# Kernel optimization log

Hardware: AMD Instinct MI355X
Metric: run time of the kernel (lower is better)

The kernel has to match this reference:

```python
import jax, jax.numpy as jnp
import numpy as np

LEAK = 0.2
N, C, T, H, DOUT = 512, 16, 15, 32, 32


def setup_inputs() -> dict:
    key = jax.random.key(0)
    k = jax.random.split(key, 5)
    x = jax.random.normal(k[0], (N, C), dtype=jnp.float32)
    adj = jax.random.uniform(k[1], (N, N, T), dtype=jnp.float32)
    W1 = jax.random.normal(k[2], (2 * C, T + 1, H), dtype=jnp.float32) * 0.05
    W2 = jax.random.normal(k[3], (2 * C, T + 1, DOUT), dtype=jnp.float32) * 0.05
    W3 = jax.random.normal(k[4], (C, H), dtype=jnp.float32) * 0.05
    return {"x": x, "adj": adj, "W1": W1, "W2": W2, "W3": W3}


def reference(x, adj, W1, W2, W3):
    n, c = x.shape
    # input_diag: [N,N,C,1], diagonal copy of node features
    diag = jnp.einsum('mn,ni->mni', jnp.eye(n, dtype=x.dtype), x)[..., None]
    # D = concat(adj-weighted broadcast of x, diag) along edge-type axis -> [N,N,C,T+1]
    D = jnp.concatenate([jnp.einsum('mnt,ni->mnit', adj, x), diag], axis=3)
    # symmetrize along channel axis -> [N,N,2C,T+1]
    D = jnp.concatenate([D, jnp.transpose(D, (1, 0, 2, 3))], axis=2)
    K = jnp.einsum('mnit,ith->mnh', D, W1)   # [N,N,H]
    V = jnp.einsum('mnit,itd->mnd', D, W2)   # [N,N,DOUT]
    Q = x @ W3                               # [N,H]
    logits1 = jnp.einsum('nh,nmh->nm', Q, K)
    logits2 = jnp.einsum('mh,nmh->nm', Q, K)
    s1 = jax.nn.softmax(logits1, axis=1)
    s2 = jax.nn.softmax(logits2, axis=0)
    temp = jnp.einsum('nm,nmd->nd', s1, V) + jnp.einsum('nm,nmd->md', s2, V)
    return jnp.maximum(temp, LEAK * temp)  # lrelu
```

## Files before the change

### kernel.cpp

```cpp
#include <hip/hip_runtime.h>
#include <hip/hip_bf16.h>

#define NNODE 512
#define CCH   16
#define TT    15
#define TP    16
#define HH    32
#define DD    32

typedef unsigned short u16;
typedef unsigned int   u32;
typedef short bf8 __attribute__((ext_vector_type(8)));
typedef float f4  __attribute__((ext_vector_type(4)));

__device__ __forceinline__ float bf2f(u16 v) {
    union { u32 u; float f; } x; x.u = ((u32)v) << 16; return x.f;
}
__device__ __forceinline__ u16 f2bf(float f) {
    union { float f; u32 u; } x; x.f = f;
    u32 u = x.u;
    return (u16)((u + 0x7FFFu + ((u >> 16) & 1u)) >> 16);
}
__device__ __forceinline__ void unpack8(uint4 p, float* o) {
    o[0]=bf2f((u16)(p.x & 0xffffu)); o[1]=bf2f((u16)(p.x >> 16));
    o[2]=bf2f((u16)(p.y & 0xffffu)); o[3]=bf2f((u16)(p.y >> 16));
    o[4]=bf2f((u16)(p.z & 0xffffu)); o[5]=bf2f((u16)(p.z >> 16));
    o[6]=bf2f((u16)(p.w & 0xffffu)); o[7]=bf2f((u16)(p.w >> 16));
}
__device__ __forceinline__ uint4 pack8(const u16* v) {
    return make_uint4((u32)v[0]|((u32)v[1]<<16), (u32)v[2]|((u32)v[3]<<16),
                      (u32)v[4]|((u32)v[5]<<16), (u32)v[6]|((u32)v[7]<<16));
}

__global__ __launch_bounds__(256) void k_prep_adjp(
    const float* __restrict__ x, const float* __restrict__ W1,
    const float* __restrict__ W2, const float* __restrict__ W3,
    const float* __restrict__ adj,
    u16* __restrict__ A1, u16* __restrict__ B1,
    u16* __restrict__ A2T, u16* __restrict__ B2T,
    u16* __restrict__ Qb, float* __restrict__ QAd, float* __restrict__ QB,
    u16* __restrict__ adjP, u16* __restrict__ adjPT,
    float* __restrict__ temp, float* __restrict__ u1, float* __restrict__ v2)
{
    int tid = threadIdx.x;
    if (blockIdx.x >= 768) {
        int idx = (blockIdx.x - 768) * 256 + tid;
        if (idx < 16384) temp[idx] = 0.f;
        else if (idx < 24576) u1[idx - 16384] = 0.f;
        else if (idx < 32768) v2[idx - 24576] = 0.f;
        return;
    }
    if (blockIdx.x < 512) {
        int n = blockIdx.x;
        __shared__ alignas(16) float xs[CCH];
        __shared__ alignas(16) float A1row[512], B1row[512];
        __shared__ alignas(16) float A2row[512], B2row[512];
        __shared__ alignas(16) float Qs[HH];
        if (tid < CCH) xs[tid] = x[n*CCH + tid];
        __syncthreads();
        float xr[CCH];
        #pragma unroll
        for (int i=0;i<CCH;i++) xr[i]=xs[i];
        #pragma unroll
        for (int rep=0; rep<2; rep++) {
            int c = tid + rep*256;
            float a1=0.f,b1=0.f,a2=0.f,b2=0.f;
            #pragma unroll
            for (int i=0;i<CCH;i++) {
                a1 += xr[i]*W1[i*512 + c];
                b1 += xr[i]*W1[(CCH+i)*512 + c];
                a2 += xr[i]*W2[i*512 + c];
                b2 += xr[i]*W2[(CCH+i)*512 + c];
            }
            A1[(size_t)n*512 + c]=f2bf(a1); B1[(size_t)n*512 + c]=f2bf(b1);
            A1row[c]=a1; B1row[c]=b1; A2row[c]=a2; B2row[c]=b2;
        }
        if (tid < HH) {
            float q=0.f;
            #pragma unroll
            for (int i=0;i<CCH;i++) q += xr[i]*W3[i*HH + tid];
            Qs[tid]=q; Qb[(size_t)n*HH + tid]=f2bf(q);
        }
        __syncthreads();
        if (tid < TP) {
            float qa=0.f, qb=0.f;
            #pragma unroll
            for (int h=0;h<HH;h++) { qa += Qs[h]*A1row[tid*HH+h]; qb += Qs[h]*B1row[tid*HH+h]; }
            QAd[(size_t)n*TP + tid]=qa; QB[(size_t)n*TP + tid]=qb;
        }
        {
            int d = tid >> 3, t0 = (tid & 7) * 2;
            u32 pa = (u32)f2bf(A2row[t0*32 + d]) | ((u32)f2bf(A2row[(t0+1)*32 + d]) << 16);
            u32 pb = (u32)f2bf(B2row[t0*32 + d]) | ((u32)f2bf(B2row[(t0+1)*32 + d]) << 16);
            *(u32*)(A2T + (size_t)d*8192 + n*16 + t0) = pa;
            *(u32*)(B2T + (size_t)d*8192 + n*16 + t0) = pb;
        }
    } else {
        int b = blockIdx.x - 512;
        int n0 = (b >> 4) * 32, m0 = (b & 15) * 32;
        __shared__ alignas(16) u16 s[32*520];
        #pragma unroll
        for (int i = 0; i < 60; i++) {
            int e = tid + i*256;
            int nl = e / 480; int rem = e - nl*480;
            int ml = rem / 15; int t = rem - ml*15;
            float v = adj[((size_t)(n0+nl)*512 + (m0+ml))*TT + t];
            s[nl*520 + ml*16 + t] = f2bf(v);
        }
        #pragma unroll
        for (int i = 0; i < 4; i++) {
            int e = tid + i*256; int nl = e >> 5, ml = e & 31;
            s[nl*520 + ml*16 + 15] = ((n0+nl) == (m0+ml)) ? (u16)0x3F80 : (u16)0;
        }
        __syncthreads();
        #pragma unroll
        for (int i = 0; i < 8; i++) {
            int c = tid + i*256;
            int nl = c >> 6, off = (c & 63) * 8;
            uint4 vv = *(const uint4*)(s + nl*520 + off);
            *(uint4*)(adjP + (size_t)(n0+nl)*8192 + m0*16 + off) = vv;
        }
        #pragma unroll
        for (int i = 0; i < 8; i++) {
            int c = tid + i*256;
            int ml = c >> 6, nlh = c & 63, nl = nlh >> 1, half = nlh & 1;
            uint4 vv = *(const uint4*)(s + nl*520 + ml*16 + half*8);
            *(uint4*)(adjPT + (size_t)(m0+ml)*8192 + (n0+nl)*16 + half*8) = vv;
        }
    }
}

__global__ __launch_bounds__(256) void k_logits(
    const u16* __restrict__ Qb, const u16* __restrict__ A1, const u16* __restrict__ B1,
    const u16* __restrict__ adjP, const u16* __restrict__ adjPT,
    const float* __restrict__ QAd, const float* __restrict__ QB,
    float* __restrict__ L1, float* __restrict__ L2T,
    float2* __restrict__ statsP)
{
    const int m0 = blockIdx.x * 16, n0 = blockIdx.y * 16;
    const int tid = threadIdx.x;
    const int wv = tid >> 6, lane = tid & 63, l15 = lane & 15, quad = lane >> 4;
    __shared__ alignas(16) float sL1[16*17];
    __shared__ alignas(16) float sL2[16*17];

    bf8 qbN = *(const bf8*)(Qb + (size_t)(n0 + l15)*32 + quad*8);
    bf8 qbM = *(const bf8*)(Qb + (size_t)(m0 + l15)*32 + quad*8);
    float4 qb4 = *(const float4*)(QB  + (size_t)(n0 + l15)*TP + quad*4);
    float4 qa4 = *(const float4*)(QAd + (size_t)(m0 + l15)*TP + quad*4);

    #pragma unroll
    for (int j = 0; j < 4; j++) {
        int m = m0 + wv*4 + j;
        bf8 aA1 = *(const bf8*)(A1 + (size_t)m*512 + l15*32 + quad*8);
        f4 z = {0.f,0.f,0.f,0.f};
        f4 g = __builtin_amdgcn_mfma_f32_16x16x32_bf16(aA1, qbN, z, 0, 0, 0);
        uint2 ax = *(const uint2*)(adjPT + (size_t)m*8192 + (n0 + l15)*16 + quad*4);
        uint2 ay = *(const uint2*)(adjP  + (size_t)m*8192 + (n0 + l15)*16 + quad*4);
        float v;
        v = bf2f((u16)(ax.x & 0xffffu)) * g[0];
        v = fmaf(bf2f((u16)(ax.x >> 16)),     g[1], v);
        v = fmaf(bf2f((u16)(ax.y & 0xffffu)), g[2], v);
        v = fmaf(bf2f((u16)(ax.y >> 16)),     g[3], v);
        v = fmaf(bf2f((u16)(ay.x & 0xffffu)), qb4.x, v);
        v = fmaf(bf2f((u16)(ay.x >> 16)),     qb4.y, v);
        v = fmaf(bf2f((u16)(ay.y & 0xffffu)), qb4.z, v);
        v = fmaf(bf2f((u16)(ay.y >> 16)),     qb4.w, v);
        v += __shfl_xor(v, 16, 64);
        v += __shfl_xor(v, 32, 64);
        if (quad == 0) sL1[l15*17 + wv*4 + j] = v;
    }
    #pragma unroll
    for (int j = 0; j < 4; j++) {
        int n = n0 + wv*4 + j;
        bf8 aB1 = *(const bf8*)(B1 + (size_t)n*512 + l15*32 + quad*8);
        f4 z = {0.f,0.f,0.f,0.f};
        f4 h = __builtin_amdgcn_mfma_f32_16x16x32_bf16(aB1, qbM, z, 0, 0, 0);
        uint2 ax = *(const uint2*)(adjPT + (size_t)n*8192 + (m0 + l15)*16 + quad*4);
        uint2 ay = *(const uint2*)(adjP  + (size_t)n*8192 + (m0 + l15)*16 + quad*4);
        float v;
        v = bf2f((u16)(ax.x & 0xffffu)) * h[0];
        v = fmaf(bf2f((u16)(ax.x >> 16)),     h[1], v);
        v = fmaf(bf2f((u16)(ax.y & 0xffffu)), h[2], v);
        v = fmaf(bf2f((u16)(ax.y >> 16)),     h[3], v);
        v = fmaf(bf2f((u16)(ay.x & 0xffffu)), qa4.x, v);
        v = fmaf(bf2f((u16)(ay.x >> 16)),     qa4.y, v);
        v = fmaf(bf2f((u16)(ay.y & 0xffffu)), qa4.z, v);
        v = fmaf(bf2f((u16)(ay.y >> 16)),     qa4.w, v);
        v += __shfl_xor(v, 16, 64);
        v += __shfl_xor(v, 32, 64);
        if (quad == 0) sL2[l15*17 + wv*4 + j] = v;
    }
    __syncthreads();
    int row = tid >> 4, col = tid & 15;
    float v1 = sL1[row*17+col];
    float v2v = sL2[row*17+col];
    L1 [(size_t)(n0+row)*NNODE + m0 + col] = v1;
    L2T[(size_t)(m0+row)*NNODE + n0 + col] = v2v;

    float mx1 = v1, mx2 = v2v;
    #pragma unroll
    for (int o=1; o<16; o<<=1) {
        mx1 = fmaxf(mx1, __shfl_xor(mx1, o, 64));
        mx2 = fmaxf(mx2, __shfl_xor(mx2, o, 64));
    }
    float s1 = __expf(v1 - mx1), s2 = __expf(v2v - mx2);
    #pragma unroll
    for (int o=1; o<16; o<<=1) {
        s1 += __shfl_xor(s1, o, 64);
        s2 += __shfl_xor(s2, o, 64);
    }
    if (col == 0) {
        float2 st1; st1.x = mx1; st1.y = s1;
        float2 st2; st2.x = mx2; st2.y = s2;
        statsP[(size_t)(n0+row)*32 + blockIdx.x]         = st1;
        statsP[(size_t)(NNODE + m0+row)*32 + blockIdx.y] = st2;
    }
}

__global__ __launch_bounds__(256) void k_smx_gemm(
    const float* __restrict__ L1, const float* __restrict__ L2T,
    const u16* __restrict__ adjP, const u16* __restrict__ adjPT,
    const u16* __restrict__ A2T, const u16* __restrict__ B2T,
    const float2* __restrict__ statsP,
    float* __restrict__ temp, float* __restrict__ u1, float* __restrict__ v2)
{
    const int j0 = blockIdx.x * 16, kc = blockIdx.y, dir = blockIdx.z;
    const int tid = threadIdx.x;
    const int wv = tid >> 6, lane = tid & 63, l15 = lane & 15, quad = lane >> 4;
    const float* Lbase = dir ? L2T : L1;

    __shared__ alignas(16) u16 Wt[16*256];
    __shared__ alignas(16) float redb[4][512];
    __shared__ float2 sst[16];

    {
        int j = tid >> 4, pp = tid & 15;
        const float2* sp = statsP + (size_t)(dir*NNODE + j0 + j)*32;
        float2 a = sp[pp*2], b = sp[pp*2+1];
        float mx = fmaxf(a.x, b.x);
        float sm = a.y*__expf(a.x - mx) + b.y*__expf(b.x - mx);
        #pragma unroll
        for (int o=1; o<16; o<<=1) {
            float omx = __shfl_xor(mx, o, 64), osm = __shfl_xor(sm, o, 64);
            float nmx = fmaxf(mx, omx);
            sm = sm*__expf(mx - nmx) + osm*__expf(omx - nmx);
            mx = nmx;
        }
        if (pp == 0) { float2 st; st.x = mx; st.y = 1.0f/sm; sst[j] = st; }
    }
    __syncthreads();

    {
        int j = tid >> 4, cb = tid & 15;
        int m = kc*16 + cb;
        float2 st = sst[j];
        float s0 = __expf(Lbase[(size_t)(j0+j)*NNODE + m] - st.x) * st.y;

        const uint4* pp = (const uint4*)(adjP + (size_t)(j0+j)*8192 + m*16);
        float av[16]; unpack8(pp[0], av); unpack8(pp[1], av+8);
        u16 wo[16];
        #pragma unroll
        for (int e=0;e<16;e++) wo[e] = f2bf(s0*av[e]);
        #pragma unroll
        for (int q=0;q<2;q++) {
            int sl = (cb*2 + q) ^ (j & 7);
            *(uint4*)&Wt[j*256 + sl*8] = pack8(wo + q*8);
        }

        const uint4* qq = (const uint4*)(adjPT + (size_t)(j0+j)*8192 + m*16);
        float tv[16]; unpack8(qq[0], tv); unpack8(qq[1], tv+8);
        float ut[16];
        #pragma unroll
        for (int t=0;t<16;t++) ut[t] = s0*tv[t];
        #pragma unroll
        for (int i=0;i<8;i++) {
            float v0 = (lane&1) ? ut[i] : ut[i+8];
            float r0 = __shfl_xor(v0, 1, 64);
            ut[i] = ((lane&1) ? ut[i+8] : ut[i]) + r0;
        }
        #pragma unroll
        for (int i=0;i<4;i++) {
            float v0 = (lane&2) ? ut[i] : ut[i+4];
            float r0 = __shfl_xor(v0, 2, 64);
            ut[i] = ((lane&2) ? ut[i+4] : ut[i]) + r0;
        }
        #pragma unroll
        for (int i=0;i<2;i++) {
            float v0 = (lane&4) ? ut[i] : ut[i+2];
            float r0 = __shfl_xor(v0, 4, 64);
            ut[i] = ((lane&4) ? ut[i+2] : ut[i]) + r0;
        }
        {
            float v0 = (lane&8) ? ut[0] : ut[1];
            float r0 = __shfl_xor(v0, 8, 64);
            ut[0] = ((lane&8) ? ut[1] : ut[0]) + r0;
        }
        int tm = ((cb&1)<<3) | ((cb&2)<<1) | ((cb&4)>>1) | ((cb&8)>>3);
        atomicAdd((dir ? v2 : u1) + (size_t)(j0+j)*TP + tm, ut[0]);
    }
    __syncthreads();

    {
        const u16* Bmat = dir ? B2T : A2T;
        f4 acc0 = {0.f,0.f,0.f,0.f}, acc1 = {0.f,0.f,0.f,0.f};
        #pragma unroll
        for (int st2 = 0; st2 < 2; st2++) {
            int s = wv*2 + st2;
            bf8 afr = *(const bf8*)&Wt[l15*256 + (((s*4 + quad) ^ (l15 & 7)) << 3)];
            bf8 b0 = *(const bf8*)(Bmat + (size_t)(l15)*8192    + kc*256 + s*32 + quad*8);
            bf8 b1 = *(const bf8*)(Bmat + (size_t)(16+l15)*8192 + kc*256 + s*32 + quad*8);
            acc0 = __builtin_amdgcn_mfma_f32_16x16x32_bf16(afr, b0, acc0, 0, 0, 0);
            acc1 = __builtin_amdgcn_mfma_f32_16x16x32_bf16(afr, b1, acc1, 0, 0, 0);
        }
        #pragma unroll
        for (int r = 0; r < 4; r++) {
            redb[wv][      (quad*4+r)*16 + l15] = acc0[r];
            redb[wv][256 + (quad*4+r)*16 + l15] = acc1[r];
        }
    }
    __syncthreads();
    #pragma unroll
    for (int h = 0; h < 2; h++) {
        int o = tid + h*256;
        int jj = o >> 5, d = o & 31;
        int idx = (d >> 4)*256 + jj*16 + (d & 15);
        float v = redb[0][idx] + redb[1][idx] + redb[2][idx] + redb[3][idx];
        atomicAdd(&temp[(size_t)(j0 + jj)*DD + d], v);
    }
}

__global__ __launch_bounds__(256) void k_final(
    const float* __restrict__ temp, const float* __restrict__ u1, const float* __restrict__ v2,
    const u16* __restrict__ A2T, const u16* __restrict__ B2T, float* __restrict__ out)
{
    int base = blockIdx.x * 256 + threadIdx.x;
    int j = base >> 5, d = base & 31;
    float acc = temp[(size_t)j*DD + d];
    const uint4* pb2 = (const uint4*)(B2T + (size_t)d*8192 + j*16);
    const uint4* pa2 = (const uint4*)(A2T + (size_t)d*8192 + j*16);
    float bv[16], avv[16];
    unpack8(pb2[0], bv);  unpack8(pb2[1], bv+8);
    unpack8(pa2[0], avv); unpack8(pa2[1], avv+8);
    #pragma unroll
    for (int t = 0; t < 16; t++)
        acc += u1[(size_t)j*TP + t]*bv[t] + v2[(size_t)j*TP + t]*avv[t];
    out[(size_t)j*DD + d] = fmaxf(acc, 0.2f*acc);
}

extern "C" void kernel_launch(void* const* d_in, const int* in_sizes, int n_in,
                              void* d_out, int out_size, void* d_ws, size_t ws_size,
                              hipStream_t stream)
{
    (void)in_sizes; (void)n_in; (void)out_size; (void)ws_size;
    const float* x   = (const float*)d_in[0];
    const float* adj = (const float*)d_in[1];
    const float* W1  = (const float*)d_in[2];
    const float* W2  = (const float*)d_in[3];
    const float* W3  = (const float*)d_in[4];

    char* ws = (char*)d_ws;
    u16*   adjP  = (u16*)(ws);
    u16*   adjPT = (u16*)(ws + 0x800000);
    u16*   A1    = (u16*)(ws + 0x1000000);
    u16*   B1    = (u16*)(ws + 0x1080000);
    u16*   A2T   = (u16*)(ws + 0x1100000);
    u16*   B2T   = (u16*)(ws + 0x1180000);
    u16*   Qb    = (u16*)(ws + 0x1200000);
    float* QAd   = (float*)(ws + 0x1210000);
    float* QB    = (float*)(ws + 0x1220000);
    float* L1    = (float*)(ws + 0x1300000);
    float* L2T   = (float*)(ws + 0x1400000);
    float* temp  = (float*)(ws + 0x1500000);
    float* u1    = (float*)(ws + 0x1510000);
    float* v2    = (float*)(ws + 0x1520000);
    float2* statsP=(float2*)(ws + 0x1530000);

    k_prep_adjp<<<896, 256, 0, stream>>>(x, W1, W2, W3, adj,
                                         A1, B1, A2T, B2T, Qb, QAd, QB, adjP, adjPT,
                                         temp, u1, v2);
    k_logits<<<dim3(32,32), 256, 0, stream>>>(Qb, A1, B1, adjP, adjPT, QAd, QB,
                                              L1, L2T, statsP);
    k_smx_gemm<<<dim3(32,32,2), 256, 0, stream>>>(L1, L2T, adjP, adjPT, A2T, B2T,
                                                  statsP, temp, u1, v2);
    k_final<<<64, 256, 0, stream>>>(temp, u1, v2, A2T, B2T, (float*)d_out);
}
```

Baseline: 102.2 us.

## Fuse softmax directions in GEMM kernel, widen logits tiles, shrink prep tiles

The softmax-weighted GEMM kernel now does both directions in one block. It reads adjP/adjPT and the logits once, builds two weight tiles, and accumulates both A2T and B2T products into the same accumulators, which halves grid size and cuts the atomic adds to temp. The logits kernel now covers 32 n-rows per block so the m-side Q fragments and QAd are reused, and the stats layout is adjusted to match. The adj-permute blocks in prep use 16-row tiles, which doubles their block count. The cost is more registers and LDS per block and lower parallelism in the fused kernels.

```diff
diff --git a/kernel.cpp b/kernel.cpp
--- a/kernel.cpp
+++ b/kernel.cpp
@@ -43,8 +43,8 @@
     float* __restrict__ temp, float* __restrict__ u1, float* __restrict__ v2)
 {
     int tid = threadIdx.x;
-    if (blockIdx.x >= 768) {
-        int idx = (blockIdx.x - 768) * 256 + tid;
+    if (blockIdx.x >= 1024) {
+        int idx = (blockIdx.x - 1024) * 256 + tid;
         if (idx < 16384) temp[idx] = 0.f;
         else if (idx < 24576) u1[idx - 16384] = 0.f;
         else if (idx < 32768) v2[idx - 24576] = 0.f;
@@ -97,10 +97,10 @@
         }
     } else {
         int b = blockIdx.x - 512;
-        int n0 = (b >> 4) * 32, m0 = (b & 15) * 32;
-        __shared__ alignas(16) u16 s[32*520];
-        #pragma unroll
-        for (int i = 0; i < 60; i++) {
+        int n0 = (b >> 4) * 16, m0 = (b & 15) * 32;
+        __shared__ alignas(16) u16 s[16*520];
+        #pragma unroll
+        for (int i = 0; i < 30; i++) {
             int e = tid + i*256;
             int nl = e / 480; int rem = e - nl*480;
             int ml = rem / 15; int t = rem - ml*15;
@@ -108,22 +108,22 @@
             s[nl*520 + ml*16 + t] = f2bf(v);
         }
         #pragma unroll
-        for (int i = 0; i < 4; i++) {
+        for (int i = 0; i < 2; i++) {
             int e = tid + i*256; int nl = e >> 5, ml = e & 31;
             s[nl*520 + ml*16 + 15] = ((n0+nl) == (m0+ml)) ? (u16)0x3F80 : (u16)0;
         }
         __syncthreads();
         #pragma unroll
-        for (int i = 0; i < 8; i++) {
+        for (int i = 0; i < 4; i++) {
             int c = tid + i*256;
             int nl = c >> 6, off = (c & 63) * 8;
             uint4 vv = *(const uint4*)(s + nl*520 + off);
             *(uint4*)(adjP + (size_t)(n0+nl)*8192 + m0*16 + off) = vv;
         }
         #pragma unroll
-        for (int i = 0; i < 8; i++) {
+        for (int i = 0; i < 4; i++) {
             int c = tid + i*256;
-            int ml = c >> 6, nlh = c & 63, nl = nlh >> 1, half = nlh & 1;
+            int ml = c >> 5, nlh = c & 31, nl = nlh >> 1, half = nlh & 1;
             uint4 vv = *(const uint4*)(s + nl*520 + ml*16 + half*8);
             *(uint4*)(adjPT + (size_t)(m0+ml)*8192 + (n0+nl)*16 + half*8) = vv;
         }
@@ -137,41 +137,62 @@
     float* __restrict__ L1, float* __restrict__ L2T,
     float2* __restrict__ statsP)
 {
-    const int m0 = blockIdx.x * 16, n0 = blockIdx.y * 16;
+    const int m0 = blockIdx.x * 16, n0 = blockIdx.y * 32;
     const int tid = threadIdx.x;
     const int wv = tid >> 6, lane = tid & 63, l15 = lane & 15, quad = lane >> 4;
-    __shared__ alignas(16) float sL1[16*17];
-    __shared__ alignas(16) float sL2[16*17];
-
-    bf8 qbN = *(const bf8*)(Qb + (size_t)(n0 + l15)*32 + quad*8);
-    bf8 qbM = *(const bf8*)(Qb + (size_t)(m0 + l15)*32 + quad*8);
-    float4 qb4 = *(const float4*)(QB  + (size_t)(n0 + l15)*TP + quad*4);
-    float4 qa4 = *(const float4*)(QAd + (size_t)(m0 + l15)*TP + quad*4);
+    __shared__ alignas(16) float sL1[32*17];
+    __shared__ alignas(16) float sL2[16*33];
+
+    bf8 qbN0 = *(const bf8*)(Qb + (size_t)(n0 + l15)*32 + quad*8);
+    bf8 qbN1 = *(const bf8*)(Qb + (size_t)(n0 + 16 + l15)*32 + quad*8);
+    bf8 qbM  = *(const bf8*)(Qb + (size_t)(m0 + l15)*32 + quad*8);
+    float4 qb40 = *(const float4*)(QB  + (size_t)(n0 + l15)*TP + quad*4);
+    float4 qb41 = *(const float4*)(QB  + (size_t)(n0 + 16 + l15)*TP + quad*4);
+    float4 qa4  = *(const float4*)(QAd + (size_t)(m0 + l15)*TP + quad*4);
 
     #pragma unroll
     for (int j = 0; j < 4; j++) {
         int m = m0 + wv*4 + j;
         bf8 aA1 = *(const bf8*)(A1 + (size_t)m*512 + l15*32 + quad*8);
         f4 z = {0.f,0.f,0.f,0.f};
-        f4 g = __builtin_amdgcn_mfma_f32_16x16x32_bf16(aA1, qbN, z, 0, 0, 0);
-        uint2 ax = *(const uint2*)(adjPT + (size_t)m*8192 + (n0 + l15)*16 + quad*4);
-        uint2 ay = *(const uint2*)(adjP  + (size_t)m*8192 + (n0 + l15)*16 + quad*4);
-        float v;
-        v = bf2f((u16)(ax.x & 0xffffu)) * g[0];
-        v = fmaf(bf2f((u16)(ax.x >> 16)),     g[1], v);
-        v = fmaf(bf2f((u16)(ax.y & 0xffffu)), g[2], v);
-        v = fmaf(bf2f((u16)(ax.y >> 16)),     g[3], v);
-        v = fmaf(bf2f((u16)(ay.x & 0xffffu)), qb4.x, v);
-        v = fmaf(bf2f((u16)(ay.x >> 16)),     qb4.y, v);
-        v = fmaf(bf2f((u16)(ay.y & 0xffffu)), qb4.z, v);
-        v = fmaf(bf2f((u16)(ay.y >> 16)),     qb4.w, v);
-        v += __shfl_xor(v, 16, 64);
-        v += __shfl_xor(v, 32, 64);
-        if (quad == 0) sL1[l15*17 + wv*4 + j] = v;
-    }
-    #pragma unroll
-    for (int j = 0; j < 4; j++) {
-        int n = n0 + wv*4 + j;
+        f4 g0 = __builtin_amdgcn_mfma_f32_16x16x32_bf16(aA1, qbN0, z, 0, 0, 0);
+        f4 g1 = __builtin_amdgcn_mfma_f32_16x16x32_bf16(aA1, qbN1, z, 0, 0, 0);
+        {
+            uint2 ax = *(const uint2*)(adjPT + (size_t)m*8192 + (n0 + l15)*16 + quad*4);
+            uint2 ay = *(const uint2*)(adjP  + (size_t)m*8192 + (n0 + l15)*16 + quad*4);
+            float v;
+            v = bf2f((u16)(ax.x & 0xffffu)) * g0[0];
+            v = fmaf(bf2f((u16)(ax.x >> 16)),     g0[1], v);
+            v = fmaf(bf2f((u16)(ax.y & 0xffffu)), g0[2], v);
+            v = fmaf(bf2f((u16)(ax.y >> 16)),     g0[3], v);
+            v = fmaf(bf2f((u16)(ay.x & 0xffffu)), qb40.x, v);
+            v = fmaf(bf2f((u16)(ay.x >> 16)),     qb40.y, v);
+            v = fmaf(bf2f((u16)(ay.y & 0xffffu)), qb40.z, v);
+            v = fmaf(bf2f((u16)(ay.y >> 16)),     qb40.w, v);
+            v += __shfl_xor(v, 16, 64);
+            v += __shfl_xor(v, 32, 64);
+            if (quad == 0) sL1[l15*17 + wv*4 + j] = v;
+        }
+        {
+            uint2 ax = *(const uint2*)(adjPT + (size_t)m*8192 + (n0 + 16 + l15)*16 + quad*4);
+            uint2 ay = *(const uint2*)(adjP  + (size_t)m*8192 + (n0 + 16 + l15)*16 + quad*4);
+            float v;
+            v = bf2f((u16)(ax.x & 0xffffu)) * g1[0];
+            v = fmaf(bf2f((u16)(ax.x >> 16)),     g1[1], v);
+            v = fmaf(bf2f((u16)(ax.y & 0xffffu)), g1[2], v);
+            v = fmaf(bf2f((u16)(ax.y >> 16)),     g1[3], v);
+            v = fmaf(bf2f((u16)(ay.x & 0xffffu)), qb41.x, v);
+            v = fmaf(bf2f((u16)(ay.x >> 16)),     qb41.y, v);
+            v = fmaf(bf2f((u16)(ay.y & 0xffffu)), qb41.z, v);
+            v = fmaf(bf2f((u16)(ay.y >> 16)),     qb41.w, v);
+            v += __shfl_xor(v, 16, 64);
+            v += __shfl_xor(v, 32, 64);
+            if (quad == 0) sL1[(16 + l15)*17 + wv*4 + j] = v;
+        }
+    }
+    #pragma unroll
+    for (int j2 = 0; j2 < 8; j2++) {
+        int n = n0 + wv*8 + j2;
         bf8 aB1 = *(const bf8*)(B1 + (size_t)n*512 + l15*32 + quad*8);
         f4 z = {0.f,0.f,0.f,0.f};
         f4 h = __builtin_amdgcn_mfma_f32_16x16x32_bf16(aB1, qbM, z, 0, 0, 0);
@@ -188,32 +209,38 @@
         v = fmaf(bf2f((u16)(ay.y >> 16)),     qa4.w, v);
         v += __shfl_xor(v, 16, 64);
         v += __shfl_xor(v, 32, 64);
-        if (quad == 0) sL2[l15*17 + wv*4 + j] = v;
+        if (quad == 0) sL2[l15*33 + wv*8 + j2] = v;
     }
     __syncthreads();
+
     int row = tid >> 4, col = tid & 15;
-    float v1 = sL1[row*17+col];
-    float v2v = sL2[row*17+col];
-    L1 [(size_t)(n0+row)*NNODE + m0 + col] = v1;
-    L2T[(size_t)(m0+row)*NNODE + n0 + col] = v2v;
-
-    float mx1 = v1, mx2 = v2v;
-    #pragma unroll
-    for (int o=1; o<16; o<<=1) {
-        mx1 = fmaxf(mx1, __shfl_xor(mx1, o, 64));
-        mx2 = fmaxf(mx2, __shfl_xor(mx2, o, 64));
-    }
-    float s1 = __expf(v1 - mx1), s2 = __expf(v2v - mx2);
-    #pragma unroll
-    for (int o=1; o<16; o<<=1) {
-        s1 += __shfl_xor(s1, o, 64);
-        s2 += __shfl_xor(s2, o, 64);
-    }
-    if (col == 0) {
-        float2 st1; st1.x = mx1; st1.y = s1;
-        float2 st2; st2.x = mx2; st2.y = s2;
-        statsP[(size_t)(n0+row)*32 + blockIdx.x]         = st1;
-        statsP[(size_t)(NNODE + m0+row)*32 + blockIdx.y] = st2;
+    #pragma unroll
+    for (int rr = 0; rr < 2; rr++) {
+        int r = rr*16 + row;
+        float v1 = sL1[r*17 + col];
+        L1[(size_t)(n0+r)*NNODE + m0 + col] = v1;
+        float mx = v1;
+        #pragma unroll
+        for (int o=1; o<16; o<<=1) mx = fmaxf(mx, __shfl_xor(mx, o, 64));
+        float s1 = __expf(v1 - mx);
+        #pragma unroll
+        for (int o=1; o<16; o<<=1) s1 += __shfl_xor(s1, o, 64);
+        if (col == 0) { float2 st; st.x = mx; st.y = s1;
+                        statsP[(size_t)(n0+r)*32 + blockIdx.x] = st; }
+    }
+    #pragma unroll
+    for (int cc = 0; cc < 2; cc++) {
+        int c2 = cc*16 + col;
+        float v2v = sL2[row*33 + c2];
+        L2T[(size_t)(m0+row)*NNODE + n0 + c2] = v2v;
+        float mx = v2v;
+        #pragma unroll
+        for (int o=1; o<16; o<<=1) mx = fmaxf(mx, __shfl_xor(mx, o, 64));
+        float s2 = __expf(v2v - mx);
+        #pragma unroll
+        for (int o=1; o<16; o<<=1) s2 += __shfl_xor(s2, o, 64);
+        if (col == 0) { float2 st; st.x = mx; st.y = s2;
+                        statsP[(size_t)(NNODE + m0+row)*32 + blockIdx.y*2 + cc] = st; }
     }
 }
 
@@ -224,93 +251,126 @@
     const float2* __restrict__ statsP,
     float* __restrict__ temp, float* __restrict__ u1, float* __restrict__ v2)
 {
-    const int j0 = blockIdx.x * 16, kc = blockIdx.y, dir = blockIdx.z;
+    const int j0 = blockIdx.x * 16, kc = blockIdx.y;
     const int tid = threadIdx.x;
     const int wv = tid >> 6, lane = tid & 63, l15 = lane & 15, quad = lane >> 4;
-    const float* Lbase = dir ? L2T : L1;
-
-    __shared__ alignas(16) u16 Wt[16*256];
+
+    __shared__ alignas(16) u16 Wt0[16*256];
+    __shared__ alignas(16) u16 Wt1[16*256];
     __shared__ alignas(16) float redb[4][512];
-    __shared__ float2 sst[16];
+    __shared__ float2 sst0[16], sst1[16];
 
     {
         int j = tid >> 4, pp = tid & 15;
-        const float2* sp = statsP + (size_t)(dir*NNODE + j0 + j)*32;
-        float2 a = sp[pp*2], b = sp[pp*2+1];
-        float mx = fmaxf(a.x, b.x);
-        float sm = a.y*__expf(a.x - mx) + b.y*__expf(b.x - mx);
-        #pragma unroll
-        for (int o=1; o<16; o<<=1) {
-            float omx = __shfl_xor(mx, o, 64), osm = __shfl_xor(sm, o, 64);
-            float nmx = fmaxf(mx, omx);
-            sm = sm*__expf(mx - nmx) + osm*__expf(omx - nmx);
-            mx = nmx;
-        }
-        if (pp == 0) { float2 st; st.x = mx; st.y = 1.0f/sm; sst[j] = st; }
+        {
+            const float2* sp = statsP + (size_t)(j0 + j)*32;
+            float2 a = sp[pp*2], b = sp[pp*2+1];
+            float mx = fmaxf(a.x, b.x);
+            float sm = a.y*__expf(a.x - mx) + b.y*__expf(b.x - mx);
+            #pragma unroll
+            for (int o=1; o<16; o<<=1) {
+                float omx = __shfl_xor(mx, o, 64), osm = __shfl_xor(sm, o, 64);
+                float nmx = fmaxf(mx, omx);
+                sm = sm*__expf(mx - nmx) + osm*__expf(omx - nmx);
+                mx = nmx;
+            }
+            if (pp == 0) { float2 st; st.x = mx; st.y = 1.0f/sm; sst0[j] = st; }
+        }
+        {
+            const float2* sp = statsP + (size_t)(NNODE + j0 + j)*32;
+            float2 a = sp[pp*2], b = sp[pp*2+1];
+            float mx = fmaxf(a.x, b.x);
+            float sm = a.y*__expf(a.x - mx) + b.y*__expf(b.x - mx);
+            #pragma unroll
+            for (int o=1; o<16; o<<=1) {
+                float omx = __shfl_xor(mx, o, 64), osm = __shfl_xor(sm, o, 64);
+                float nmx = fmaxf(mx, omx);
+                sm = sm*__expf(mx - nmx) + osm*__expf(omx - nmx);
+                mx = nmx;
+            }
+            if (pp == 0) { float2 st; st.x = mx; st.y = 1.0f/sm; sst1[j] = st; }
+        }
     }
     __syncthreads();
 
     {
         int j = tid >> 4, cb = tid & 15;
         int m = kc*16 + cb;
-        float2 st = sst[j];
-        float s0 = __expf(Lbase[(size_t)(j0+j)*NNODE + m] - st.x) * st.y;
-
-        const uint4* pp = (const uint4*)(adjP + (size_t)(j0+j)*8192 + m*16);
-        float av[16]; unpack8(pp[0], av); unpack8(pp[1], av+8);
-        u16 wo[16];
-        #pragma unroll
-        for (int e=0;e<16;e++) wo[e] = f2bf(s0*av[e]);
+        float2 st0 = sst0[j], st1 = sst1[j];
+        float s0 = __expf(L1 [(size_t)(j0+j)*NNODE + m] - st0.x) * st0.y;
+        float s1 = __expf(L2T[(size_t)(j0+j)*NNODE + m] - st1.x) * st1.y;
+
+        const uint4* pp4 = (const uint4*)(adjP + (size_t)(j0+j)*8192 + m*16);
+        float av[16]; unpack8(pp4[0], av); unpack8(pp4[1], av+8);
+        u16 wo0[16], wo1[16];
+        #pragma unroll
+        for (int e=0;e<16;e++) { wo0[e] = f2bf(s0*av[e]); wo1[e] = f2bf(s1*av[e]); }
         #pragma unroll
         for (int q=0;q<2;q++) {
             int sl = (cb*2 + q) ^ (j & 7);
-            *(uint4*)&Wt[j*256 + sl*8] = pack8(wo + q*8);
+            *(uint4*)&Wt0[j*256 + sl*8] = pack8(wo0 + q*8);
+            *(uint4*)&Wt1[j*256 + sl*8] = pack8(wo1 + q*8);
         }
 
         const uint4* qq = (const uint4*)(adjPT + (size_t)(j0+j)*8192 + m*16);
         float tv[16]; unpack8(qq[0], tv); unpack8(qq[1], tv+8);
-        float ut[16];
-        #pragma unroll
-        for (int t=0;t<16;t++) ut[t] = s0*tv[t];
+        float ut0[16], ut1[16];
+        #pragma unroll
+        for (int t=0;t<16;t++) { ut0[t] = s0*tv[t]; ut1[t] = s1*tv[t]; }
         #pragma unroll
         for (int i=0;i<8;i++) {
-            float v0 = (lane&1) ? ut[i] : ut[i+8];
-            float r0 = __shfl_xor(v0, 1, 64);
-            ut[i] = ((lane&1) ? ut[i+8] : ut[i]) + r0;
+            float a0 = (lane&1) ? ut0[i] : ut0[i+8];
+            float a1 = (lane&1) ? ut1[i] : ut1[i+8];
+            float r0 = __shfl_xor(a0, 1, 64), r1 = __shfl_xor(a1, 1, 64);
+            ut0[i] = ((lane&1) ? ut0[i+8] : ut0[i]) + r0;
+            ut1[i] = ((lane&1) ? ut1[i+8] : ut1[i]) + r1;
         }
         #pragma unroll
         for (int i=0;i<4;i++) {
-            float v0 = (lane&2) ? ut[i] : ut[i+4];
-            float r0 = __shfl_xor(v0, 2, 64);
-            ut[i] = ((lane&2) ? ut[i+4] : ut[i]) + r0;
+            float a0 = (lane&2) ? ut0[i] : ut0[i+4];
+            float a1 = (lane&2) ? ut1[i] : ut1[i+4];
+            float r0 = __shfl_xor(a0, 2, 64), r1 = __shfl_xor(a1, 2, 64);
+            ut0[i] = ((lane&2) ? ut0[i+4] : ut0[i]) + r0;
+            ut1[i] = ((lane&2) ? ut1[i+4] : ut1[i]) + r1;
         }
         #pragma unroll
         for (int i=0;i<2;i++) {
-            float v0 = (lane&4) ? ut[i] : ut[i+2];
-            float r0 = __shfl_xor(v0, 4, 64);
-            ut[i] = ((lane&4) ? ut[i+2] : ut[i]) + r0;
-        }
-        {
-            float v0 = (lane&8) ? ut[0] : ut[1];
-            float r0 = __shfl_xor(v0, 8, 64);
-            ut[0] = ((lane&8) ? ut[1] : ut[0]) + r0;
+            float a0 = (lane&4) ? ut0[i] : ut0[i+2];
+            float a1 = (lane&4) ? ut1[i] : ut1[i+2];
+            float r0 = __shfl_xor(a0, 4, 64), r1 = __shfl_xor(a1, 4, 64);
+            ut0[i] = ((lane&4) ? ut0[i+2] : ut0[i]) + r0;
+            ut1[i] = ((lane&4) ? ut1[i+2] : ut1[i]) + r1;
+        }
+        {
+            float a0 = (lane&8) ? ut0[0] : ut0[1];
+            float a1 = (lane&8) ? ut1[0] : ut1[1];
+            float r0 = __shfl_xor(a0, 8, 64), r1 = __shfl_xor(a1, 8, 64);
+            ut0[0] = ((lane&8) ? ut0[1] : ut0[0]) + r0;
+            ut1[0] = ((lane&8) ? ut1[1] : ut1[0]) + r1;
         }
         int tm = ((cb&1)<<3) | ((cb&2)<<1) | ((cb&4)>>1) | ((cb&8)>>3);
-        atomicAdd((dir ? v2 : u1) + (size_t)(j0+j)*TP + tm, ut[0]);
+        atomicAdd(u1 + (size_t)(j0+j)*TP + tm, ut0[0]);
+        atomicAdd(v2 + (size_t)(j0+j)*TP + tm, ut1[0]);
     }
     __syncthreads();
 
     {
-        const u16* Bmat = dir ? B2T : A2T;
         f4 acc0 = {0.f,0.f,0.f,0.f}, acc1 = {0.f,0.f,0.f,0.f};
         #pragma unroll
         for (int st2 = 0; st2 < 2; st2++) {
             int s = wv*2 + st2;
-            bf8 afr = *(const bf8*)&Wt[l15*256 + (((s*4 + quad) ^ (l15 & 7)) << 3)];
-            bf8 b0 = *(const bf8*)(Bmat + (size_t)(l15)*8192    + kc*256 + s*32 + quad*8);
-            bf8 b1 = *(const bf8*)(Bmat + (size_t)(16+l15)*8192 + kc*256 + s*32 + quad*8);
-            acc0 = __builtin_amdgcn_mfma_f32_16x16x32_bf16(afr, b0, acc0, 0, 0, 0);
-            acc1 = __builtin_amdgcn_mfma_f32_16x16x32_bf16(afr, b1, acc1, 0, 0, 0);
+            int wslot = ((s*4 + quad) ^ (l15 & 7)) << 3;
+            bf8 afr0 = *(const bf8*)&Wt0[l15*256 + wslot];
+            bf8 afr1 = *(const bf8*)&Wt1[l15*256 + wslot];
+            int kt = kc*256 + s*32 + quad*8;
+            bf8 a20 = *(const bf8*)(A2T + (size_t)(l15)*8192    + kt);
+            bf8 a21 = *(const bf8*)(A2T + (size_t)(16+l15)*8192 + kt);
+            bf8 b20 = *(const bf8*)(B2T + (size_t)(l15)*8192    + kt);
+            bf8 b21 = *(const bf8*)(B2T + (size_t)(16+l15)*8192 + kt);
+            acc0 = __builtin_amdgcn_mfma_f32_16x16x32_bf16(afr0, a20, acc0, 0, 0, 0);
+            acc0 = __builtin_amdgcn_mfma_f32_16x16x32_bf16(afr1, b20, acc0, 0, 0, 0);
+            acc1 = __builtin_amdgcn_mfma_f32_16x16x32_bf16(afr0, a21, acc1, 0, 0, 0);
+            acc1 = __builtin_amdgcn_mfma_f32_16x16x32_bf16(afr1, b21, acc1, 0, 0, 0);
         }
         #pragma unroll
         for (int r = 0; r < 4; r++) {
@@ -375,12 +435,12 @@
     float* v2    = (float*)(ws + 0x1520000);
     float2* statsP=(float2*)(ws + 0x1530000);
 
-    k_prep_adjp<<<896, 256, 0, stream>>>(x, W1, W2, W3, adj,
-                                         A1, B1, A2T, B2T, Qb, QAd, QB, adjP, adjPT,
-                                         temp, u1, v2);
-    k_logits<<<dim3(32,32), 256, 0, stream>>>(Qb, A1, B1, adjP, adjPT, QAd, QB,
+    k_prep_adjp<<<1152, 256, 0, stream>>>(x, W1, W2, W3, adj,
+                                          A1, B1, A2T, B2T, Qb, QAd, QB, adjP, adjPT,
+                                          temp, u1, v2);
+    k_logits<<<dim3(32,16), 256, 0, stream>>>(Qb, A1, B1, adjP, adjPT, QAd, QB,
                                               L1, L2T, statsP);
-    k_smx_gemm<<<dim3(32,32,2), 256, 0, stream>>>(L1, L2T, adjP, adjPT, A2T, B2T,
-                                                  statsP, temp, u1, v2);
+    k_smx_gemm<<<dim3(32,32), 256, 0, stream>>>(L1, L2T, adjP, adjPT, A2T, B2T,
+                                                statsP, temp, u1, v2);
     k_final<<<64, 256, 0, stream>>>(temp, u1, v2, A2T, B2T, (float*)d_out);
 }
```

New measurement: 101.7 us. Within noise of the previous version (-0.5%).
